# Performance work log

Measured on AMD Instinct MI355X. Metric: run time of the kernel, lower is better.

Reference implementation:

```python
import jax, jax.numpy as jnp
import numpy as np

N_ARY = 2
H = 128
X_SIZE = 128
DEPTH = 18  # levels in complete binary tree; n = 2^DEPTH - 1 = 262143 nodes


def setup_inputs() -> dict:
    key = jax.random.key(0)
    k0, k1, k2, k3 = jax.random.split(key, 4)
    n = (N_ARY ** DEPTH - 1) // (N_ARY - 1)
    x = jax.random.normal(k0, (n, X_SIZE), jnp.float32)
    W_w = jax.random.normal(k1, (2 * H, X_SIZE), jnp.float32) * 0.05
    W_b = jnp.zeros((2 * H,), jnp.float32)
    U_f = jax.random.normal(k2, (H, N_ARY * H), jnp.float32) * 0.05
    U_hc = jax.random.normal(k3, (H, N_ARY * H), jnp.float32) * 0.05
    return {"x": x, "W_w": W_w, "W_b": W_b, "U_f": U_f, "U_hc": U_hc, "depth": DEPTH}


def reference(x, W_w, W_b, U_f, U_hc, depth):
    """Tree-structured single-forget-gate MGU on a complete N_ARY tree.

    Node i (level-order) has children N_ARY*i+1 .. N_ARY*i+N_ARY. Levels are
    processed bottom-up (leaves first), matching DGL topological prop_nodes.
    """
    n_ary, h_size = N_ARY, H
    n = x.shape[0]
    wx = x @ W_w.T + W_b                      # [n, 2h]
    w_hc_x = wx[:, :h_size]                   # candidate pre-activation part
    w_f_x = wx[:, h_size:]                    # forget-gate pre-activation part
    h = jnp.zeros((n, h_size), x.dtype)
    for lvl in range(depth - 1, -1, -1):
        start = (n_ary ** lvl - 1) // (n_ary - 1)
        size = n_ary ** lvl
        whc = w_hc_x[start:start + size]
        wf = w_f_x[start:start + size]
        if lvl == depth - 1:
            # leaves: mailbox empty -> f_in = 0, h_cat = 0, h_sum = 0
            f = jax.nn.sigmoid(wf)
            new_h = (1.0 - f) * jnp.tanh(whc)
        else:
            # children of [start, start+size) occupy the contiguous next-level block
            child_start = n_ary * start + 1
            h_child = h[child_start:child_start + size * n_ary]
            h_child = h_child.reshape(size, n_ary, h_size)
            h_cat = h_child.reshape(size, n_ary * h_size)
            f = jax.nn.sigmoid(h_cat @ U_f.T + wf)
            f_rep = jnp.tile(f, (1, n_ary))
            h_cand = jnp.tanh(whc + (f_rep * h_cat) @ U_hc.T)
            new_h = f * h_child.sum(axis=1) + (1.0 - f) * h_cand
        h = h.at[start:start + size].set(new_h)
    return h
```

## Files before the change

kernel.cpp:

```cpp
#include <hip/hip_runtime.h>
#include <cmath>

#define NT 256

#define NTOT   262143
#define NINT   131071

#define WHC_OFF   0
#define WF_OFF    (NINT * 128)
#define UFT_OFF   (2 * NINT * 128)
#define UHCT_OFF  (UFT_OFF + 32768)
#define PKWW_OFF  (UHCT_OFF + 32768)
#define PKUF_OFF  (PKWW_OFF + 98304)
#define PKUHC_OFF (PKUF_OFF + 98304)
#define WS_FLOATS (PKUHC_OFF + 98304)
#define WS_BYTES  ((size_t)WS_FLOATS * 4)

#define PA_PACK 0x120100
#define PB_PACK 0x102010

typedef __attribute__((ext_vector_type(8))) short short8v;
typedef __attribute__((ext_vector_type(4))) float f32x4;

__device__ __forceinline__ float sigmoid_(float v) {
    return 1.0f / (1.0f + expf(-v));
}

__device__ __forceinline__ void split3(float a, unsigned &t0, unsigned &t1, unsigned &t2) {
    unsigned u0 = __float_as_uint(a) & 0xffff0000u;
    float f0 = __uint_as_float(u0);
    float r1 = a - f0;
    unsigned u1 = __float_as_uint(r1) & 0xffff0000u;
    float f1 = __uint_as_float(u1);
    float r2 = r1 - f1;
    unsigned u2 = __float_as_uint(r2) & 0xffff0000u;
    t0 = u0 >> 16; t1 = u1 >> 16; t2 = u2 >> 16;
}
__device__ __forceinline__ float bf2f(unsigned hbits) {
    return __uint_as_float(hbits << 16);
}

__global__ __launch_bounds__(NT) void prep_pack(
    const float* __restrict__ Ww, const float* __restrict__ Uf,
    const float* __restrict__ Uhc, float* __restrict__ ws)
{
    int t = blockIdx.x * NT + threadIdx.x;
    if (t < 32768) { int k = t >> 7, j = t & 127; ws[UFT_OFF + t] = Uf[j * 256 + k]; return; }
    t -= 32768;
    if (t < 32768) { int k = t >> 7, j = t & 127; ws[UHCT_OFF + t] = Uhc[j * 256 + k]; return; }
    t -= 32768;

    const float* src; int term; uint4* dst; int q;
    if (t < 24576) {
        q = t;
        int l = q & 63, j = (q >> 6) & 15, s = q >> 10;
        int p = s >> 2, ks = s & 3;
        term = (PB_PACK >> (p * 4)) & 3;
        int kb = ks * 32 + (l >> 4) * 8, col = j * 16 + (l & 15);
        src = Ww + col * 128 + kb;
        dst = (uint4*)(ws + PKWW_OFF);
    } else if (t < 49152) {
        q = t - 24576;
        int l = q & 63, j = (q >> 6) & 7, s = q >> 9;
        int p = s >> 3, ks = s & 7;
        term = (PB_PACK >> (p * 4)) & 3;
        int kb = ks * 32 + (l >> 4) * 8, col = j * 16 + (l & 15);
        src = Uf + col * 256 + kb;
        dst = (uint4*)(ws + PKUF_OFF);
    } else if (t < 73728) {
        q = t - 49152;
        int l = q & 63, j = (q >> 6) & 7, s = q >> 9;
        int p = s >> 3, ks = s & 7;
        term = (PB_PACK >> (p * 4)) & 3;
        int kb = ks * 32 + (l >> 4) * 8, col = j * 16 + (l & 15);
        src = Uhc + col * 256 + kb;
        dst = (uint4*)(ws + PKUHC_OFF);
    } else return;

    unsigned hv[8];
#pragma unroll
    for (int e = 0; e < 8; ++e) {
        unsigned a, b, c; split3(src[e], a, b, c);
        hv[e] = (term == 0) ? a : (term == 1 ? b : c);
    }
    uint4 o;
    o.x = hv[0] | (hv[1] << 16); o.y = hv[2] | (hv[3] << 16);
    o.z = hv[4] | (hv[5] << 16); o.w = hv[6] | (hv[7] << 16);
    dst[q] = o;
}

#define LOADC(srcbase) { const uint4* s_ = (srcbase); \
    nx0 = s_[tid]; nx1 = s_[tid + 512]; nx2 = s_[tid + 1024]; nx3 = s_[tid + 1536]; }
#define WRITEC(dstbase) { uint4* d_ = (dstbase); \
    d_[tid] = nx0; d_[tid + 512] = nx1; d_[tid + 1024] = nx2; d_[tid + 1536] = nx3; }

__global__ __launch_bounds__(512) void wx_mfma4(
    const float* __restrict__ x, const float* __restrict__ ws_all,
    const float* __restrict__ Wb, float* __restrict__ ws, float* __restrict__ h)
{
    __shared__ short As[128 * 384];
    __shared__ uint4 sBb[2][2048];
    char* Asb = (char*)As;
    const int tid = threadIdx.x;
    const int nbase = blockIdx.x * 128;
    const uint4* pkb = (const uint4*)(ws_all + PKWW_OFF);

    uint4 nx0, nx1, nx2, nx3;
    LOADC(pkb);

    for (int i = 0; i < 8; ++i) {
        int idx = i * 512 + tid;
        int m = idx >> 5, g = idx & 31;
        int node = nbase + m; if (node > NTOT - 1) node = NTOT - 1;
        float4 v = *(const float4*)(x + (size_t)node * 128 + g * 4);
        unsigned a0[4], a1[4], a2[4];
        split3(v.x, a0[0], a1[0], a2[0]); split3(v.y, a0[1], a1[1], a2[1]);
        split3(v.z, a0[2], a1[2], a2[2]); split3(v.w, a0[3], a1[3], a2[3]);
        int ks = g >> 3, kg = (g >> 1) & 3, hw = (g & 1) * 8;
        int kss = ks ^ ((m >> 2) & 3), kgs = kg ^ (m & 3);
        char* base = Asb + m * 768 + kgs * 16 + hw;
        *(uint2*)(base + ((0 * 4 + kss) << 6)) = make_uint2(a0[0] | (a0[1] << 16), a0[2] | (a0[3] << 16));
        *(uint2*)(base + ((1 * 4 + kss) << 6)) = make_uint2(a1[0] | (a1[1] << 16), a1[2] | (a1[3] << 16));
        *(uint2*)(base + ((2 * 4 + kss) << 6)) = make_uint2(a2[0] | (a2[1] << 16), a2[2] | (a2[3] << 16));
    }
    WRITEC(&sBb[0][0]);
    __syncthreads();

    const int lane = tid & 63, wv = tid >> 6;
    const int li = lane & 15, kg = lane >> 4;
    const int mf = wv * 16 + li;
    const int mswz = (mf >> 2) & 3;
    const char* arbase = Asb + mf * 768 + ((kg ^ (mf & 3)) << 4);

    f32x4 acc[16];
#pragma unroll
    for (int j = 0; j < 16; ++j) acc[j] = (f32x4){0.f, 0.f, 0.f, 0.f};

    int cur = 0;
#pragma unroll 1
    for (int c = 0; c < 12; ++c) {
        if (c < 11) LOADC(pkb + (c + 1) * 2048);
        const int p = c >> 1, hh = c & 1;
        const int spA = (PA_PACK >> (p * 4)) & 3;
        const short8v* sBs = (const short8v*)&sBb[cur][0];
#pragma unroll
        for (int ks2 = 0; ks2 < 2; ++ks2) {
            int ks = hh * 2 + ks2;
            short8v a = *(const short8v*)(arbase + ((spA * 4 + (ks ^ mswz)) << 6));
#pragma unroll
            for (int j = 0; j < 16; ++j)
                acc[j] = __builtin_amdgcn_mfma_f32_16x16x32_bf16(a, sBs[(ks2 * 16 + j) * 64 + lane], acc[j], 0, 0, 0);
        }
        if (c < 11) WRITEC(&sBb[cur ^ 1][0]);
        __syncthreads();
        cur ^= 1;
    }

    float* whcw = ws + WHC_OFF;
    float* wfw  = ws + WF_OFF;
    const int rbase = wv * 16 + kg * 4;
#pragma unroll
    for (int r = 0; r < 4; ++r) {
        int node = nbase + rbase + r;
        if (node >= NTOT) continue;
        if (node < NINT) {
#pragma unroll
            for (int j = 0; j < 16; ++j) {
                int col = j * 16 + li;
                float v = acc[j][r] + Wb[col];
                if (col < 128) whcw[(size_t)node * 128 + col] = v;
                else           wfw [(size_t)node * 128 + col - 128] = v;
            }
        } else {
#pragma unroll
            for (int j = 0; j < 8; ++j) {
                int col = j * 16 + li;
                float hc = acc[j][r] + Wb[col];
                float wf = acc[j + 8][r] + Wb[col + 128];
                float f = sigmoid_(wf);
                h[(size_t)node * 128 + col] = (1.0f - f) * tanhf(hc);
            }
        }
    }
}

__global__ __launch_bounds__(512) void lvl_fused(
    const float* __restrict__ ws_all, float* __restrict__ h, int start)
{
    __shared__ short As[64 * 768];
    __shared__ uint4 sBb[2][2048];
    char* Asb = (char*)As;
    float* f_lds = (float*)&sBb[0][0];
    const int tid = threadIdx.x;
    const int s0 = start + blockIdx.x * 64;
    const float* hbase = h + ((size_t)2 * s0 + 1) * 128;
    const uint4* ufpk  = (const uint4*)(ws_all + PKUF_OFF);
    const uint4* uhcpk = (const uint4*)(ws_all + PKUHC_OFF);
    const float* wfw   = ws_all + WF_OFF;
    const float* whcw  = ws_all + WHC_OFF;

    uint4 nx0, nx1, nx2, nx3;
    LOADC(ufpk);

    for (int i = 0; i < 8; ++i) {
        int idx = i * 512 + tid;
        int m = idx >> 6, g = idx & 63;
        float4 v = *(const float4*)(hbase + m * 256 + g * 4);
        unsigned a0[4], a1[4], a2[4];
        split3(v.x, a0[0], a1[0], a2[0]); split3(v.y, a0[1], a1[1], a2[1]);
        split3(v.z, a0[2], a1[2], a2[2]); split3(v.w, a0[3], a1[3], a2[3]);
        int ks = g >> 3, kg = (g >> 1) & 3, hw = (g & 1) * 8;
        int kss = ks ^ ((m >> 2) & 7), kgs = kg ^ (m & 3);
        char* base = Asb + m * 1536 + kgs * 16 + hw;
        *(uint2*)(base + ((0 * 8 + kss) << 6)) = make_uint2(a0[0] | (a0[1] << 16), a0[2] | (a0[3] << 16));
        *(uint2*)(base + ((1 * 8 + kss) << 6)) = make_uint2(a1[0] | (a1[1] << 16), a1[2] | (a1[3] << 16));
        *(uint2*)(base + ((2 * 8 + kss) << 6)) = make_uint2(a2[0] | (a2[1] << 16), a2[2] | (a2[3] << 16));
    }
    WRITEC(&sBb[0][0]);
    __syncthreads();

    const int lane = tid & 63, wv = tid >> 6;
    const int li = lane & 15, kg = lane >> 4;
    const int rt = wv & 3, jh = wv >> 2;
    const int mf = rt * 16 + li;
    const int mswz = (mf >> 2) & 7;
    const char* arbase = Asb + mf * 1536 + ((kg ^ (mf & 3)) << 4);
    const int rbase = rt * 16 + kg * 4;

    f32x4 acc[4];
#pragma unroll
    for (int j = 0; j < 4; ++j) acc[j] = (f32x4){0.f, 0.f, 0.f, 0.f};

    int cur = 0;
#pragma unroll 1
    for (int c = 0; c < 12; ++c) {
        if (c < 11) LOADC(ufpk + (c + 1) * 2048);
        const int p = c >> 1, hh = c & 1;
        const int spA = (PA_PACK >> (p * 4)) & 3;
        const short8v* sBs = (const short8v*)&sBb[cur][0];
#pragma unroll
        for (int ks2 = 0; ks2 < 4; ++ks2) {
            int ks = hh * 4 + ks2;
            short8v a = *(const short8v*)(arbase + ((spA * 8 + (ks ^ mswz)) << 6));
#pragma unroll
            for (int jj = 0; jj < 4; ++jj)
                acc[jj] = __builtin_amdgcn_mfma_f32_16x16x32_bf16(a, sBs[(ks2 * 8 + jh * 4 + jj) * 64 + lane], acc[jj], 0, 0, 0);
        }
        if (c < 11) WRITEC(&sBb[cur ^ 1][0]);
        __syncthreads();
        cur ^= 1;
    }
    float freg[4][4];
#pragma unroll
    for (int jj = 0; jj < 4; ++jj)
#pragma unroll
        for (int r = 0; r < 4; ++r) {
            int col = (jh * 4 + jj) * 16 + li;
            size_t gn = (size_t)(s0 + rbase + r);
            float f = sigmoid_(acc[jj][r] + wfw[gn * 128 + col]);
            freg[jj][r] = f;
            f_lds[(rbase + r) * 128 + col] = f;
        }
    __syncthreads();

    LOADC(uhcpk);
    for (int i = 0; i < 4; ++i) {
        int idx = i * 512 + tid;
        int kgr = idx & 3, ksr = (idx >> 2) & 7, m = idx >> 5;
        int kss = ksr ^ ((m >> 2) & 7);
        int kgs = kgr ^ (m & 3);
        char* base = Asb + m * 1536 + (kgs << 4);
        uint4 g0 = *(uint4*)(base + ((0 * 8 + kss) << 6));
        uint4 g1 = *(uint4*)(base + ((1 * 8 + kss) << 6));
        uint4 g2 = *(uint4*)(base + ((2 * 8 + kss) << 6));
        unsigned w0[4] = {g0.x, g0.y, g0.z, g0.w};
        unsigned w1[4] = {g1.x, g1.y, g1.z, g1.w};
        unsigned w2[4] = {g2.x, g2.y, g2.z, g2.w};
        unsigned o0[4] = {0, 0, 0, 0}, o1[4] = {0, 0, 0, 0}, o2[4] = {0, 0, 0, 0};
#pragma unroll
        for (int e = 0; e < 8; ++e) {
            unsigned h0 = (e & 1) ? (w0[e >> 1] >> 16) : (w0[e >> 1] & 0xffffu);
            unsigned h1 = (e & 1) ? (w1[e >> 1] >> 16) : (w1[e >> 1] & 0xffffu);
            unsigned h2 = (e & 1) ? (w2[e >> 1] >> 16) : (w2[e >> 1] & 0xffffu);
            float a = bf2f(h0) + bf2f(h1) + bf2f(h2);
            int kph = ksr * 32 + kgr * 8 + e;
            float pv = a * f_lds[m * 128 + (kph & 127)];
            unsigned s0_, s1_, s2_; split3(pv, s0_, s1_, s2_);
            o0[e >> 1] |= s0_ << ((e & 1) * 16);
            o1[e >> 1] |= s1_ << ((e & 1) * 16);
            o2[e >> 1] |= s2_ << ((e & 1) * 16);
        }
        *(uint4*)(base + ((0 * 8 + kss) << 6)) = make_uint4(o0[0], o0[1], o0[2], o0[3]);
        *(uint4*)(base + ((1 * 8 + kss) << 6)) = make_uint4(o1[0], o1[1], o1[2], o1[3]);
        *(uint4*)(base + ((2 * 8 + kss) << 6)) = make_uint4(o2[0], o2[1], o2[2], o2[3]);
    }
    __syncthreads();
    WRITEC(&sBb[0][0]);
    __syncthreads();

    f32x4 acc2[4];
#pragma unroll
    for (int j = 0; j < 4; ++j) acc2[j] = (f32x4){0.f, 0.f, 0.f, 0.f};

    cur = 0;
#pragma unroll 1
    for (int c = 0; c < 12; ++c) {
        if (c < 11) LOADC(uhcpk + (c + 1) * 2048);
        const int p = c >> 1, hh = c & 1;
        const int spA = (PA_PACK >> (p * 4)) & 3;
        const short8v* sBs = (const short8v*)&sBb[cur][0];
#pragma unroll
        for (int ks2 = 0; ks2 < 4; ++ks2) {
            int ks = hh * 4 + ks2;
            short8v a = *(const short8v*)(arbase + ((spA * 8 + (ks ^ mswz)) << 6));
#pragma unroll
            for (int jj = 0; jj < 4; ++jj)
                acc2[jj] = __builtin_amdgcn_mfma_f32_16x16x32_bf16(a, sBs[(ks2 * 8 + jh * 4 + jj) * 64 + lane], acc2[jj], 0, 0, 0);
        }
        if (c < 11) WRITEC(&sBb[cur ^ 1][0]);
        __syncthreads();
        cur ^= 1;
    }

#pragma unroll
    for (int jj = 0; jj < 4; ++jj)
#pragma unroll
        for (int r = 0; r < 4; ++r) {
            int col = (jh * 4 + jj) * 16 + li;
            size_t gn = (size_t)(s0 + rbase + r);
            float f = freg[jj][r];
            float whcv = whcw[gn * 128 + col];
            float c1 = h[(2 * gn + 1) * 128 + col];
            float c2 = h[(2 * gn + 2) * 128 + col];
            float t = tanhf(acc2[jj][r] + whcv);
            h[gn * 128 + col] = f * (c1 + c2) + (1.0f - f) * t;
        }
}

__global__ __launch_bounds__(NT) void tail_kernel(
    const float* __restrict__ ws_all, float* __restrict__ h)
{
    __shared__ __align__(16) float bufA[64 * 128];
    __shared__ __align__(16) float bufB[32 * 128];
    __shared__ __align__(16) float sF[8 * 128];
    const float* uft  = ws_all + UFT_OFF;
    const float* uhct = ws_all + UHCT_OFF;
    const float* whcw = ws_all + WHC_OFF;
    const float* wfw  = ws_all + WF_OFF;

    const int tid = threadIdx.x;
    const int jq = tid & 31;  const int j0 = jq << 2;
    const int iq = tid >> 5;

    {
        const float4* hg = (const float4*)(h + (size_t)63 * 128);
        float4* b4 = (float4*)bufA;
        for (int idx = tid; idx < 64 * 32; idx += NT) b4[idx] = hg[idx];
    }
    __syncthreads();

    float* child = bufA;
    float* cur   = bufB;

    for (int lvl = 5; lvl >= 0; --lvl) {
        const int start = (1 << lvl) - 1;
        const int size  = 1 << lvl;
        for (int pass = 0; pass < size; pass += 8) {
            const int ni = pass + iq;
            const bool act = (ni < size);
            float f[4] = {0.f, 0.f, 0.f, 0.f};
            if (act) {
                const float* hc = child + ni * 256;
                float fv[4] = {0.f, 0.f, 0.f, 0.f};
                for (int k = 0; k < 256; k += 4) {
#pragma unroll
                    for (int u = 0; u < 4; ++u) {
                        float av = hc[k + u];
                        float4 w = *(const float4*)&uft[(size_t)(k + u) * 128 + j0];
                        fv[0] = fmaf(w.x, av, fv[0]);
                        fv[1] = fmaf(w.y, av, fv[1]);
                        fv[2] = fmaf(w.z, av, fv[2]);
                        fv[3] = fmaf(w.w, av, fv[3]);
                    }
                }
                const int gn = start + ni;
                float4 wfv = *(const float4*)&wfw[(size_t)gn * 128 + j0];
                const float* wfp = (const float*)&wfv;
#pragma unroll
                for (int j = 0; j < 4; ++j) {
                    f[j] = sigmoid_(fv[j] + wfp[j]);
                    sF[iq * 128 + j0 + j] = f[j];
                }
            }
            __syncthreads();
            if (act) {
                const float* hc = child + ni * 256;
                const float* fr = sF + iq * 128;
                float cv[4] = {0.f, 0.f, 0.f, 0.f};
                for (int k = 0; k < 256; k += 4) {
#pragma unroll
                    for (int u = 0; u < 4; ++u) {
                        float av = hc[k + u] * fr[(k + u) & 127];
                        float4 w = *(const float4*)&uhct[(size_t)(k + u) * 128 + j0];
                        cv[0] = fmaf(w.x, av, cv[0]);
                        cv[1] = fmaf(w.y, av, cv[1]);
                        cv[2] = fmaf(w.z, av, cv[2]);
                        cv[3] = fmaf(w.w, av, cv[3]);
                    }
                }
                const int gn = start + ni;
                float4 whcv = *(const float4*)&whcw[(size_t)gn * 128 + j0];
                const float* wp = (const float*)&whcv;
                float4 o;
                float* op = (float*)&o;
#pragma unroll
                for (int j = 0; j < 4; ++j) {
                    float hsum = hc[j0 + j] + hc[128 + j0 + j];
                    float t = tanhf(cv[j] + wp[j]);
                    op[j] = f[j] * hsum + (1.0f - f[j]) * t;
                }
                *(float4*)&cur[ni * 128 + j0] = o;
                *(float4*)&h[(size_t)gn * 128 + j0] = o;
            }
            __syncthreads();
        }
        float* t = child; child = cur; cur = t;
    }
}


__global__ __launch_bounds__(NT) void fb_leaf(
    const float* __restrict__ x, const float* __restrict__ Ww,
    const float* __restrict__ Wb, float* __restrict__ h, int start, int size)
{
    __shared__ float sA[32 * 128];
    __shared__ float sW[16 * 260];
    const int tid = threadIdx.x;
    const int nbase = blockIdx.x * 32;
    const int s0 = start + nbase;
    const int nb = min(32, size - nbase);
    const int jq = tid & 31, iq = tid >> 5;
    const int j0 = jq << 2, i0 = iq << 2;
    {
        const float4* xg = (const float4*)(x + (size_t)s0 * 128);
        float4* sA4 = (float4*)sA;
        for (int idx = tid; idx < nb * 32; idx += NT) sA4[idx] = xg[idx];
    }
    float whc[4][4], wf[4][4];
#pragma unroll
    for (int j = 0; j < 4; ++j)
#pragma unroll
        for (int i = 0; i < 4; ++i) { whc[j][i] = 0.f; wf[j][i] = 0.f; }
    for (int k0 = 0; k0 < 128; k0 += 16) {
        __syncthreads();
        const float4* Wg = (const float4*)Ww;
        for (int idx = tid; idx < 256 * 4; idx += NT) {
            int j2 = idx >> 2, kq = idx & 3;
            float4 v = Wg[j2 * 32 + (k0 >> 2) + kq];
            int kb = kq << 2;
            sW[(kb + 0) * 260 + j2] = v.x; sW[(kb + 1) * 260 + j2] = v.y;
            sW[(kb + 2) * 260 + j2] = v.z; sW[(kb + 3) * 260 + j2] = v.w;
        }
        __syncthreads();
#pragma unroll
        for (int kk = 0; kk < 16; kk += 4) {
            float4 a4[4];
#pragma unroll
            for (int i = 0; i < 4; ++i)
                a4[i] = ((const float4*)sA)[(i0 + i) * 32 + ((k0 + kk) >> 2)];
#pragma unroll
            for (int u = 0; u < 4; ++u) {
                int k = kk + u;
                float4 w0 = *((const float4*)&sW[k * 260 + j0]);
                float4 w1 = *((const float4*)&sW[k * 260 + 128 + j0]);
                const float* w0p = (const float*)&w0;
                const float* w1p = (const float*)&w1;
#pragma unroll
                for (int i = 0; i < 4; ++i) {
                    float av = ((const float*)&a4[i])[u];
#pragma unroll
                    for (int j = 0; j < 4; ++j) {
                        whc[j][i] = fmaf(w0p[j], av, whc[j][i]);
                        wf[j][i]  = fmaf(w1p[j], av, wf[j][i]);
                    }
                }
            }
        }
    }
#pragma unroll
    for (int i = 0; i < 4; ++i) {
        if (i0 + i < nb) {
            float4 o; float* op = (float*)&o;
#pragma unroll
            for (int j = 0; j < 4; ++j) {
                float f = sigmoid_(wf[j][i] + Wb[128 + j0 + j]);
                op[j] = (1.0f - f) * tanhf(whc[j][i] + Wb[j0 + j]);
            }
            *(float4*)&h[((size_t)(s0 + i0 + i)) * 128 + j0] = o;
        }
    }
}

__global__ __launch_bounds__(NT) void fb_internal(
    const float* __restrict__ x, const float* __restrict__ Ww,
    const float* __restrict__ Wb, const float* __restrict__ Uf,
    const float* __restrict__ Uhc, float* __restrict__ h, int start, int size)
{
    __shared__ float sA[32 * 256];
    __shared__ float sW[4224];
    const int tid = threadIdx.x;
    const int nbase = blockIdx.x * 32;
    const int s0 = start + nbase;
    const int nb = min(32, size - nbase);
    const int jq = tid & 31, iq = tid >> 5;
    const int j0 = jq << 2, i0 = iq << 2;
    {
        const float4* xg = (const float4*)(x + (size_t)s0 * 128);
        float4* sA4 = (float4*)sA;
        for (int idx = tid; idx < nb * 32; idx += NT) sA4[idx] = xg[idx];
    }
    float whc[4][4], wf[4][4];
#pragma unroll
    for (int j = 0; j < 4; ++j)
#pragma unroll
        for (int i = 0; i < 4; ++i) { whc[j][i] = 0.f; wf[j][i] = 0.f; }
    for (int k0 = 0; k0 < 128; k0 += 16) {
        __syncthreads();
        const float4* Wg = (const float4*)Ww;
        for (int idx = tid; idx < 256 * 4; idx += NT) {
            int j2 = idx >> 2, kq = idx & 3;
            float4 v = Wg[j2 * 32 + (k0 >> 2) + kq];
            int kb = kq << 2;
            sW[(kb + 0) * 260 + j2] = v.x; sW[(kb + 1) * 260 + j2] = v.y;
            sW[(kb + 2) * 260 + j2] = v.z; sW[(kb + 3) * 260 + j2] = v.w;
        }
        __syncthreads();
#pragma unroll
        for (int kk = 0; kk < 16; kk += 4) {
            float4 a4[4];
#pragma unroll
            for (int i = 0; i < 4; ++i)
                a4[i] = ((const float4*)sA)[(i0 + i) * 32 + ((k0 + kk) >> 2)];
#pragma unroll
            for (int u = 0; u < 4; ++u) {
                int k = kk + u;
                float4 w0 = *((const float4*)&sW[k * 260 + j0]);
                float4 w1 = *((const float4*)&sW[k * 260 + 128 + j0]);
                const float* w0p = (const float*)&w0;
                const float* w1p = (const float*)&w1;
#pragma unroll
                for (int i = 0; i < 4; ++i) {
                    float av = ((const float*)&a4[i])[u];
#pragma unroll
                    for (int j = 0; j < 4; ++j) {
                        whc[j][i] = fmaf(w0p[j], av, whc[j][i]);
                        wf[j][i]  = fmaf(w1p[j], av, wf[j][i]);
                    }
                }
            }
        }
    }
#pragma unroll
    for (int j = 0; j < 4; ++j) {
        float bhc = Wb[j0 + j], bf = Wb[128 + j0 + j];
#pragma unroll
        for (int i = 0; i < 4; ++i) { whc[j][i] += bhc; wf[j][i] += bf; }
    }
    __syncthreads();
    {
        const float4* hg = (const float4*)(h + ((size_t)2 * s0 + 1) * 128);
        float4* sA4 = (float4*)sA;
        for (int idx = tid; idx < nb * 64; idx += NT) sA4[idx] = hg[idx];
    }
    float fv[4][4];
#pragma unroll
    for (int j = 0; j < 4; ++j)
#pragma unroll
        for (int i = 0; i < 4; ++i) fv[j][i] = 0.f;
    for (int k0 = 0; k0 < 256; k0 += 32) {
        __syncthreads();
        const float4* Ug = (const float4*)Uf;
        for (int idx = tid; idx < 128 * 8; idx += NT) {
            int j2 = idx >> 3, kq = idx & 7;
            float4 v = Ug[j2 * 64 + (k0 >> 2) + kq];
            int kb = kq << 2;
            sW[(kb + 0) * 132 + j2] = v.x; sW[(kb + 1) * 132 + j2] = v.y;
            sW[(kb + 2) * 132 + j2] = v.z; sW[(kb + 3) * 132 + j2] = v.w;
        }
        __syncthreads();
#pragma unroll
        for (int kk = 0; kk < 32; kk += 4) {
            float4 a4[4];
#pragma unroll
            for (int i = 0; i < 4; ++i)
                a4[i] = ((const float4*)sA)[(i0 + i) * 64 + ((k0 + kk) >> 2)];
#pragma unroll
            for (int u = 0; u < 4; ++u) {
                int k = kk + u;
                float4 w = *((const float4*)&sW[k * 132 + j0]);
                const float* wp = (const float*)&w;
#pragma unroll
                for (int i = 0; i < 4; ++i) {
                    float av = ((const float*)&a4[i])[u];
#pragma unroll
                    for (int j = 0; j < 4; ++j)
                        fv[j][i] = fmaf(wp[j], av, fv[j][i]);
                }
            }
        }
    }
#pragma unroll
    for (int j = 0; j < 4; ++j)
#pragma unroll
        for (int i = 0; i < 4; ++i)
            fv[j][i] = sigmoid_(fv[j][i] + wf[j][i]);
    __syncthreads();
    float hs[4][4];
#pragma unroll
    for (int i = 0; i < 4; ++i) {
        float4* row = (float4*)&sA[(i0 + i) * 256];
        float4 c0 = row[jq], c1 = row[32 + jq];
        hs[0][i] = c0.x + c1.x; hs[1][i] = c0.y + c1.y;
        hs[2][i] = c0.z + c1.z; hs[3][i] = c0.w + c1.w;
        c0.x *= fv[0][i]; c0.y *= fv[1][i]; c0.z *= fv[2][i]; c0.w *= fv[3][i];
        c1.x *= fv[0][i]; c1.y *= fv[1][i]; c1.z *= fv[2][i]; c1.w *= fv[3][i];
        row[jq] = c0; row[32 + jq] = c1;
    }
    float cv[4][4];
#pragma unroll
    for (int j = 0; j < 4; ++j)
#pragma unroll
        for (int i = 0; i < 4; ++i) cv[j][i] = 0.f;
    for (int k0 = 0; k0 < 256; k0 += 32) {
        __syncthreads();
        const float4* Ug = (const float4*)Uhc;
        for (int idx = tid; idx < 128 * 8; idx += NT) {
            int j2 = idx >> 3, kq = idx & 7;
            float4 v = Ug[j2 * 64 + (k0 >> 2) + kq];
            int kb = kq << 2;
            sW[(kb + 0) * 132 + j2] = v.x; sW[(kb + 1) * 132 + j2] = v.y;
            sW[(kb + 2) * 132 + j2] = v.z; sW[(kb + 3) * 132 + j2] = v.w;
        }
        __syncthreads();
#pragma unroll
        for (int kk = 0; kk < 32; kk += 4) {
            float4 a4[4];
#pragma unroll
            for (int i = 0; i < 4; ++i)
                a4[i] = ((const float4*)sA)[(i0 + i) * 64 + ((k0 + kk) >> 2)];
#pragma unroll
            for (int u = 0; u < 4; ++u) {
                int k = kk + u;
                float4 w = *((const float4*)&sW[k * 132 + j0]);
                const float* wp = (const float*)&w;
#pragma unroll
                for (int i = 0; i < 4; ++i) {
                    float av = ((const float*)&a4[i])[u];
#pragma unroll
                    for (int j = 0; j < 4; ++j)
                        cv[j][i] = fmaf(wp[j], av, cv[j][i]);
                }
            }
        }
    }
#pragma unroll
    for (int i = 0; i < 4; ++i) {
        if (i0 + i < nb) {
            float4 o; float* op = (float*)&o;
#pragma unroll
            for (int j = 0; j < 4; ++j) {
                float t = tanhf(cv[j][i] + whc[j][i]);
                op[j] = fv[j][i] * hs[j][i] + (1.0f - fv[j][i]) * t;
            }
            *(float4*)&h[((size_t)(s0 + i0 + i)) * 128 + j0] = o;
        }
    }
}


extern "C" void kernel_launch(void* const* d_in, const int* in_sizes, int n_in,
                              void* d_out, int out_size, void* d_ws, size_t ws_size,
                              hipStream_t stream)
{
    (void)in_sizes; (void)n_in; (void)out_size;
    const float* x   = (const float*)d_in[0];
    const float* Ww  = (const float*)d_in[1];
    const float* Wb  = (const float*)d_in[2];
    const float* Uf  = (const float*)d_in[3];
    const float* Uhc = (const float*)d_in[4];
    float* h = (float*)d_out;
    const int depth = 18;

    if (ws_size >= WS_BYTES) {
        float* ws = (float*)d_ws;
        prep_pack<<<544, NT, 0, stream>>>(Ww, Uf, Uhc, ws);
        wx_mfma4<<<2048, 512, 0, stream>>>(x, ws, Wb, ws, h);
        for (int lvl = 16; lvl >= 6; --lvl)
            lvl_fused<<<1 << (lvl - 6), 512, 0, stream>>>(ws, h, (1 << lvl) - 1);
        tail_kernel<<<1, NT, 0, stream>>>(ws, h);
    } else {
        {
            int lvl = depth - 1;
            int start = (1 << lvl) - 1, size = 1 << lvl;
            fb_leaf<<<(size + 31) / 32, NT, 0, stream>>>(x, Ww, Wb, h, start, size);
        }
        for (int lvl = depth - 2; lvl >= 0; --lvl) {
            int start = (1 << lvl) - 1, size = 1 << lvl;
            fb_internal<<<(size + 31) / 32, NT, 0, stream>>>(x, Ww, Wb, Uf, Uhc, h, start, size);
        }
    }
}
```

Baseline: 832.1 us.

## Split level kernel into forget-gate and candidate GEMMs with 128-row tiles

Changes the wx GEMM warp tiling so each wave computes two row tiles over half the columns, reusing each B fragment twice and routing the forget-gate half through LDS for the leaf epilogue. Replaces the fused 64-row per-level kernel with two 128-row kernels: one computes the sigmoid forget gate in place in the workspace, the next forms f*h children and the candidate GEMM. The goal is better MFMA operand reuse and larger tiles. The cost is twice as many launches per level, a global round trip for f, and half as many blocks on the small levels.

```diff
diff --git a/kernel.cpp b/kernel.cpp
--- a/kernel.cpp
+++ b/kernel.cpp
@@ -94,7 +94,7 @@
 #define WRITEC(dstbase) { uint4* d_ = (dstbase); \
     d_[tid] = nx0; d_[tid + 512] = nx1; d_[tid + 1024] = nx2; d_[tid + 1536] = nx3; }
 
-__global__ __launch_bounds__(512) void wx_mfma4(
+__global__ __launch_bounds__(512) void wx_mfma5(
     const float* __restrict__ x, const float* __restrict__ ws_all,
     const float* __restrict__ Wb, float* __restrict__ ws, float* __restrict__ h)
 {
@@ -128,13 +128,17 @@
 
     const int lane = tid & 63, wv = tid >> 6;
     const int li = lane & 15, kg = lane >> 4;
-    const int mf = wv * 16 + li;
-    const int mswz = (mf >> 2) & 3;
-    const char* arbase = Asb + mf * 768 + ((kg ^ (mf & 3)) << 4);
-
-    f32x4 acc[16];
-#pragma unroll
-    for (int j = 0; j < 16; ++j) acc[j] = (f32x4){0.f, 0.f, 0.f, 0.f};
+    const int rg = wv & 3, jh = wv >> 2;
+    const int mf0 = rg * 32 + li, mf1 = mf0 + 16;
+    const int mswz0 = (mf0 >> 2) & 3, mswz1 = (mf1 >> 2) & 3;
+    const char* arbase0 = Asb + mf0 * 768 + ((kg ^ (mf0 & 3)) << 4);
+    const char* arbase1 = Asb + mf1 * 768 + ((kg ^ (mf1 & 3)) << 4);
+
+    f32x4 acc[2][8];
+#pragma unroll
+    for (int rt = 0; rt < 2; ++rt)
+#pragma unroll
+        for (int j = 0; j < 8; ++j) acc[rt][j] = (f32x4){0.f, 0.f, 0.f, 0.f};
 
     int cur = 0;
 #pragma unroll 1
@@ -146,10 +150,14 @@
 #pragma unroll
         for (int ks2 = 0; ks2 < 2; ++ks2) {
             int ks = hh * 2 + ks2;
-            short8v a = *(const short8v*)(arbase + ((spA * 4 + (ks ^ mswz)) << 6));
-#pragma unroll
-            for (int j = 0; j < 16; ++j)
-                acc[j] = __builtin_amdgcn_mfma_f32_16x16x32_bf16(a, sBs[(ks2 * 16 + j) * 64 + lane], acc[j], 0, 0, 0);
+            short8v a0 = *(const short8v*)(arbase0 + ((spA * 4 + (ks ^ mswz0)) << 6));
+            short8v a1 = *(const short8v*)(arbase1 + ((spA * 4 + (ks ^ mswz1)) << 6));
+#pragma unroll
+            for (int jj = 0; jj < 8; ++jj) {
+                short8v b = sBs[(ks2 * 16 + jh * 8 + jj) * 64 + lane];
+                acc[0][jj] = __builtin_amdgcn_mfma_f32_16x16x32_bf16(a0, b, acc[0][jj], 0, 0, 0);
+                acc[1][jj] = __builtin_amdgcn_mfma_f32_16x16x32_bf16(a1, b, acc[1][jj], 0, 0, 0);
+            }
         }
         if (c < 11) WRITEC(&sBb[cur ^ 1][0]);
         __syncthreads();
@@ -158,30 +166,230 @@
 
     float* whcw = ws + WHC_OFF;
     float* wfw  = ws + WF_OFF;
-    const int rbase = wv * 16 + kg * 4;
-#pragma unroll
-    for (int r = 0; r < 4; ++r) {
-        int node = nbase + rbase + r;
-        if (node >= NTOT) continue;
-        if (node < NINT) {
-#pragma unroll
-            for (int j = 0; j < 16; ++j) {
-                int col = j * 16 + li;
-                float v = acc[j][r] + Wb[col];
-                if (col < 128) whcw[(size_t)node * 128 + col] = v;
-                else           wfw [(size_t)node * 128 + col - 128] = v;
-            }
-        } else {
-#pragma unroll
-            for (int j = 0; j < 8; ++j) {
-                int col = j * 16 + li;
-                float hc = acc[j][r] + Wb[col];
-                float wf = acc[j + 8][r] + Wb[col + 128];
-                float f = sigmoid_(wf);
-                h[(size_t)node * 128 + col] = (1.0f - f) * tanhf(hc);
-            }
-        }
-    }
+    float* sF = (float*)&sBb[0][0];
+    if (jh == 1) {
+#pragma unroll
+        for (int rt = 0; rt < 2; ++rt)
+#pragma unroll
+            for (int jj = 0; jj < 8; ++jj) {
+                int colr = jj * 16 + li;
+                float bia = Wb[128 + colr];
+#pragma unroll
+                for (int r = 0; r < 4; ++r) {
+                    int row = rg * 32 + rt * 16 + kg * 4 + r;
+                    sF[row * 128 + colr] = acc[rt][jj][r] + bia;
+                }
+            }
+    }
+    __syncthreads();
+
+#pragma unroll
+    for (int rt = 0; rt < 2; ++rt)
+#pragma unroll
+        for (int r = 0; r < 4; ++r) {
+            int row = rg * 32 + rt * 16 + kg * 4 + r;
+            int node = nbase + row;
+            if (node >= NTOT) continue;
+            if (node < NINT) {
+                if (jh == 0) {
+#pragma unroll
+                    for (int jj = 0; jj < 8; ++jj) {
+                        int col = jj * 16 + li;
+                        whcw[(size_t)node * 128 + col] = acc[rt][jj][r] + Wb[col];
+                    }
+                } else {
+#pragma unroll
+                    for (int jj = 0; jj < 8; ++jj) {
+                        int col = jj * 16 + li;
+                        wfw[(size_t)node * 128 + col] = acc[rt][jj][r] + Wb[128 + col];
+                    }
+                }
+            } else if (jh == 0) {
+#pragma unroll
+                for (int jj = 0; jj < 8; ++jj) {
+                    int col = jj * 16 + li;
+                    float hc = acc[rt][jj][r] + Wb[col];
+                    float f = sigmoid_(sF[row * 128 + col]);
+                    h[(size_t)node * 128 + col] = (1.0f - f) * tanhf(hc);
+                }
+            }
+        }
+}
+
+__global__ __launch_bounds__(512) void b1_128(
+    const float* __restrict__ ws_all, float* __restrict__ ws,
+    const float* __restrict__ h, int start)
+{
+    __shared__ short As[128 * 384];
+    __shared__ uint4 sBb[2][2048];
+    char* Asb = (char*)As;
+    const int tid = threadIdx.x;
+    const int s0 = start + blockIdx.x * 128;
+    const uint4* ufpk = (const uint4*)(ws_all + PKUF_OFF);
+    float* wfw = ws + WF_OFF;
+
+    const int lane = tid & 63, wv = tid >> 6;
+    const int li = lane & 15, kg = lane >> 4;
+    const int rg = wv & 3, jh = wv >> 2;
+    const int mf0 = rg * 32 + li, mf1 = mf0 + 16;
+    const int mswz0 = (mf0 >> 2) & 3, mswz1 = (mf1 >> 2) & 3;
+    const char* arbase0 = Asb + mf0 * 768 + ((kg ^ (mf0 & 3)) << 4);
+    const char* arbase1 = Asb + mf1 * 768 + ((kg ^ (mf1 & 3)) << 4);
+
+    f32x4 acc[2][4];
+#pragma unroll
+    for (int rt = 0; rt < 2; ++rt)
+#pragma unroll
+        for (int j = 0; j < 4; ++j) acc[rt][j] = (f32x4){0.f, 0.f, 0.f, 0.f};
+
+    uint4 nx0, nx1, nx2, nx3;
+    int cur = 0;
+#pragma unroll 1
+    for (int half = 0; half < 2; ++half) {
+        LOADC(ufpk + (size_t)(half * 4) * 512);
+        __syncthreads();
+        for (int i = 0; i < 8; ++i) {
+            int idx = i * 512 + tid;
+            int m = idx >> 5, g = idx & 31;
+            int cn = 2 * (s0 + m) + 1 + half;
+            float4 v = *(const float4*)(h + (size_t)cn * 128 + g * 4);
+            unsigned a0[4], a1[4], a2[4];
+            split3(v.x, a0[0], a1[0], a2[0]); split3(v.y, a0[1], a1[1], a2[1]);
+            split3(v.z, a0[2], a1[2], a2[2]); split3(v.w, a0[3], a1[3], a2[3]);
+            int ks = g >> 3, kgr = (g >> 1) & 3, hw = (g & 1) * 8;
+            int kss = ks ^ ((m >> 2) & 3), kgs = kgr ^ (m & 3);
+            char* base = Asb + m * 768 + kgs * 16 + hw;
+            *(uint2*)(base + ((0 * 4 + kss) << 6)) = make_uint2(a0[0] | (a0[1] << 16), a0[2] | (a0[3] << 16));
+            *(uint2*)(base + ((1 * 4 + kss) << 6)) = make_uint2(a1[0] | (a1[1] << 16), a1[2] | (a1[3] << 16));
+            *(uint2*)(base + ((2 * 4 + kss) << 6)) = make_uint2(a2[0] | (a2[1] << 16), a2[2] | (a2[3] << 16));
+        }
+        WRITEC(&sBb[cur][0]);
+        __syncthreads();
+#pragma unroll 1
+        for (int p = 0; p < 6; ++p) {
+            if (p < 5) LOADC(ufpk + (size_t)((p + 1) * 8 + half * 4) * 512);
+            const int spA = (PA_PACK >> (p * 4)) & 3;
+            const short8v* sBs = (const short8v*)&sBb[cur][0];
+#pragma unroll
+            for (int ks = 0; ks < 4; ++ks) {
+                short8v a0 = *(const short8v*)(arbase0 + ((spA * 4 + (ks ^ mswz0)) << 6));
+                short8v a1 = *(const short8v*)(arbase1 + ((spA * 4 + (ks ^ mswz1)) << 6));
+#pragma unroll
+                for (int jj = 0; jj < 4; ++jj) {
+                    short8v b = sBs[(ks * 8 + jh * 4 + jj) * 64 + lane];
+                    acc[0][jj] = __builtin_amdgcn_mfma_f32_16x16x32_bf16(a0, b, acc[0][jj], 0, 0, 0);
+                    acc[1][jj] = __builtin_amdgcn_mfma_f32_16x16x32_bf16(a1, b, acc[1][jj], 0, 0, 0);
+                }
+            }
+            if (p < 5) WRITEC(&sBb[cur ^ 1][0]);
+            __syncthreads();
+            cur ^= 1;
+        }
+    }
+
+#pragma unroll
+    for (int rt = 0; rt < 2; ++rt)
+#pragma unroll
+        for (int jj = 0; jj < 4; ++jj) {
+            int col = jh * 64 + jj * 16 + li;
+#pragma unroll
+            for (int r = 0; r < 4; ++r) {
+                size_t gn = (size_t)(s0 + rg * 32 + rt * 16 + kg * 4 + r);
+                float wf = wfw[gn * 128 + col];
+                wfw[gn * 128 + col] = sigmoid_(acc[rt][jj][r] + wf);
+            }
+        }
+}
+
+__global__ __launch_bounds__(512) void b2_128(
+    const float* __restrict__ ws_all, float* __restrict__ h, int start)
+{
+    __shared__ short As[128 * 384];
+    __shared__ uint4 sBb[2][2048];
+    char* Asb = (char*)As;
+    const int tid = threadIdx.x;
+    const int s0 = start + blockIdx.x * 128;
+    const uint4* uhcpk = (const uint4*)(ws_all + PKUHC_OFF);
+    const float* fw   = ws_all + WF_OFF;
+    const float* whcw = ws_all + WHC_OFF;
+
+    const int lane = tid & 63, wv = tid >> 6;
+    const int li = lane & 15, kg = lane >> 4;
+    const int rg = wv & 3, jh = wv >> 2;
+    const int mf0 = rg * 32 + li, mf1 = mf0 + 16;
+    const int mswz0 = (mf0 >> 2) & 3, mswz1 = (mf1 >> 2) & 3;
+    const char* arbase0 = Asb + mf0 * 768 + ((kg ^ (mf0 & 3)) << 4);
+    const char* arbase1 = Asb + mf1 * 768 + ((kg ^ (mf1 & 3)) << 4);
+
+    f32x4 acc[2][4];
+#pragma unroll
+    for (int rt = 0; rt < 2; ++rt)
+#pragma unroll
+        for (int j = 0; j < 4; ++j) acc[rt][j] = (f32x4){0.f, 0.f, 0.f, 0.f};
+
+    uint4 nx0, nx1, nx2, nx3;
+    int cur = 0;
+#pragma unroll 1
+    for (int half = 0; half < 2; ++half) {
+        LOADC(uhcpk + (size_t)(half * 4) * 512);
+        __syncthreads();
+        for (int i = 0; i < 8; ++i) {
+            int idx = i * 512 + tid;
+            int m = idx >> 5, g = idx & 31;
+            int cn = 2 * (s0 + m) + 1 + half;
+            float4 v = *(const float4*)(h + (size_t)cn * 128 + g * 4);
+            float4 f4 = *(const float4*)(fw + (size_t)(s0 + m) * 128 + g * 4);
+            v.x *= f4.x; v.y *= f4.y; v.z *= f4.z; v.w *= f4.w;
+            unsigned a0[4], a1[4], a2[4];
+            split3(v.x, a0[0], a1[0], a2[0]); split3(v.y, a0[1], a1[1], a2[1]);
+            split3(v.z, a0[2], a1[2], a2[2]); split3(v.w, a0[3], a1[3], a2[3]);
+            int ks = g >> 3, kgr = (g >> 1) & 3, hw = (g & 1) * 8;
+            int kss = ks ^ ((m >> 2) & 3), kgs = kgr ^ (m & 3);
+            char* base = Asb + m * 768 + kgs * 16 + hw;
+            *(uint2*)(base + ((0 * 4 + kss) << 6)) = make_uint2(a0[0] | (a0[1] << 16), a0[2] | (a0[3] << 16));
+            *(uint2*)(base + ((1 * 4 + kss) << 6)) = make_uint2(a1[0] | (a1[1] << 16), a1[2] | (a1[3] << 16));
+            *(uint2*)(base + ((2 * 4 + kss) << 6)) = make_uint2(a2[0] | (a2[1] << 16), a2[2] | (a2[3] << 16));
+        }
+        WRITEC(&sBb[cur][0]);
+        __syncthreads();
+#pragma unroll 1
+        for (int p = 0; p < 6; ++p) {
+            if (p < 5) LOADC(uhcpk + (size_t)((p + 1) * 8 + half * 4) * 512);
+            const int spA = (PA_PACK >> (p * 4)) & 3;
+            const short8v* sBs = (const short8v*)&sBb[cur][0];
+#pragma unroll
+            for (int ks = 0; ks < 4; ++ks) {
+                short8v a0 = *(const short8v*)(arbase0 + ((spA * 4 + (ks ^ mswz0)) << 6));
+                short8v a1 = *(const short8v*)(arbase1 + ((spA * 4 + (ks ^ mswz1)) << 6));
+#pragma unroll
+                for (int jj = 0; jj < 4; ++jj) {
+                    short8v b = sBs[(ks * 8 + jh * 4 + jj) * 64 + lane];
+                    acc[0][jj] = __builtin_amdgcn_mfma_f32_16x16x32_bf16(a0, b, acc[0][jj], 0, 0, 0);
+                    acc[1][jj] = __builtin_amdgcn_mfma_f32_16x16x32_bf16(a1, b, acc[1][jj], 0, 0, 0);
+                }
+            }
+            if (p < 5) WRITEC(&sBb[cur ^ 1][0]);
+            __syncthreads();
+            cur ^= 1;
+        }
+    }
+
+#pragma unroll
+    for (int rt = 0; rt < 2; ++rt)
+#pragma unroll
+        for (int jj = 0; jj < 4; ++jj) {
+            int col = jh * 64 + jj * 16 + li;
+#pragma unroll
+            for (int r = 0; r < 4; ++r) {
+                size_t gn = (size_t)(s0 + rg * 32 + rt * 16 + kg * 4 + r);
+                float f = fw[gn * 128 + col];
+                float whcv = whcw[gn * 128 + col];
+                float c1 = h[(2 * gn + 1) * 128 + col];
+                float c2 = h[(2 * gn + 2) * 128 + col];
+                float t = tanhf(acc[rt][jj][r] + whcv);
+                h[gn * 128 + col] = f * (c1 + c2) + (1.0f - f) * t;
+            }
+        }
 }
 
 __global__ __launch_bounds__(512) void lvl_fused(
@@ -694,9 +902,14 @@
     if (ws_size >= WS_BYTES) {
         float* ws = (float*)d_ws;
         prep_pack<<<544, NT, 0, stream>>>(Ww, Uf, Uhc, ws);
-        wx_mfma4<<<2048, 512, 0, stream>>>(x, ws, Wb, ws, h);
-        for (int lvl = 16; lvl >= 6; --lvl)
-            lvl_fused<<<1 << (lvl - 6), 512, 0, stream>>>(ws, h, (1 << lvl) - 1);
+        wx_mfma5<<<2048, 512, 0, stream>>>(x, ws, Wb, ws, h);
+        for (int lvl = 16; lvl >= 7; --lvl) {
+            int start = (1 << lvl) - 1;
+            int grid  = 1 << (lvl - 7);
+            b1_128<<<grid, 512, 0, stream>>>(ws, ws, h, start);
+            b2_128<<<grid, 512, 0, stream>>>(ws, h, start);
+        }
+        lvl_fused<<<1, 512, 0, stream>>>(ws, h, 63);
         tail_kernel<<<1, NT, 0, stream>>>(ws, h);
     } else {
         {
```

New measurement: 1.097 ms. 31.8% more time.
